# Optimization experiments

Hardware: AMD Instinct MI355X
Metric: run time of the kernel (lower is better)

The kernel has to match this reference:

```python
import jax, jax.numpy as jnp
import numpy as np

B, F, N = 16, 64, 32768
C0, C1, C2 = 64, 16, 1
TOP_K = 64
EPS = 1e-5


def setup_inputs() -> dict:
    key = jax.random.key(0)
    ks = jax.random.split(key, 6)
    def rn(k, shape, scale=1.0):
        return jax.random.normal(k, shape, dtype=jnp.float32) * scale
    return {
        "sortvec": rn(ks[0], (B, 1, F, N)),
        "input": rn(ks[1], (B, F, N)),
        # conv0: kernel (F,1), in=1, out=64 -> weight reduces to [C0, F]
        "w0": rn(ks[2], (C0, F), np.sqrt(2.0 / F)), "b0": jnp.zeros((C0,), jnp.float32),
        "w1": rn(ks[3], (C1, C0), np.sqrt(2.0 / C0)), "b1": jnp.zeros((C1,), jnp.float32),
        "w2": rn(ks[4], (C2, C1), np.sqrt(2.0 / C1)), "b2": jnp.zeros((C2,), jnp.float32),
        "g0": jnp.ones((C0,), jnp.float32), "bt0": jnp.zeros((C0,), jnp.float32),
        "g1": jnp.ones((C1,), jnp.float32), "bt1": jnp.zeros((C1,), jnp.float32),
        "g2": jnp.ones((C2,), jnp.float32), "bt2": jnp.zeros((C2,), jnp.float32),
    }


def _bn_relu(x, g, b):
    # training-mode BatchNorm2d over (B, N) per channel; x: [B, C, N]
    mu = jnp.mean(x, axis=(0, 2), keepdims=True)
    var = jnp.var(x, axis=(0, 2), keepdims=True)
    return jax.nn.relu((x - mu) * jax.lax.rsqrt(var + EPS) * g[None, :, None] + b[None, :, None])


def reference(sortvec, input, w0, b0, w1, b1, w2, b2, g0, bt0, g1, bt1, g2, bt2):
    # conv0 with kernel (F,1) collapses the feature axis: [B,1,F,N] -> [B,C0,N]
    x = jnp.einsum('bfn,of->bon', sortvec[:, 0], w0) + b0[None, :, None]
    x = _bn_relu(x, g0, bt0)
    x = _bn_relu(jnp.einsum('bcn,oc->bon', x, w1) + b1[None, :, None], g1, bt1)
    score = _bn_relu(jnp.einsum('bcn,oc->bon', x, w2) + b2[None, :, None], g2, bt2)  # [B,1,N]
    _, idx = jax.lax.top_k(score[:, 0], TOP_K)                                        # [B,K]
    sorted_input = jnp.take_along_axis(input, idx[:, None, :], axis=2)                # [B,F,K]
    sorted_score = jnp.take_along_axis(score, idx[:, None, :], axis=2)                # [B,1,K]
    feat = jnp.concatenate([sorted_input, sorted_score], axis=1)                      # [B,F+1,K]
    return feat, idx
```

## Files before the change

### kernel.cpp

```cpp
#include <hip/hip_runtime.h>


constexpr int   B_   = 16;
constexpr int   N_   = 32768;
constexpr int   K_   = 64;
constexpr long long S_ = (long long)B_ * N_;
constexpr float EPS_ = 1e-5f;

constexpr int NB0   = 1024;
constexpr int NB1   = 2048;
constexpr int NB2   = 128;
constexpr int T64   = 8192;
constexpr int NBINS = 4096;
constexpr int CAP   = 1024;

__device__ __forceinline__ unsigned key_map(float f) {
  unsigned u = __float_as_uint(f);
  return (u & 0x80000000u) ? ~u : (u | 0x80000000u);
}

__global__ __launch_bounds__(256) void k_prep(const float* __restrict__ w0,
                                              const float* __restrict__ w1,
                                              float* __restrict__ w0T,
                                              float* __restrict__ w1T) {
  int t = threadIdx.x;
  for (int e = t; e < 64 * 64; e += 256) {
    int o = e >> 6, f = e & 63;
    w0T[f * 64 + o] = w0[e];
  }
  for (int e = t; e < 16 * 64; e += 256) {
    int o = e >> 6, c = e & 63;
    w1T[c * 16 + o] = w1[e];
  }
}

__global__ __launch_bounds__(256) void k_stat0(const float* __restrict__ sv,
                                               const float* __restrict__ w0T,
                                               const float* __restrict__ b0,
                                               float* __restrict__ p0) {
  __shared__ float svt[64][64];
  const int t  = threadIdx.x;
  const int p  = t & 63;
  const int cg = __builtin_amdgcn_readfirstlane(t >> 6);

  float bb[16];
#pragma unroll
  for (int j = 0; j < 16; ++j) bb[j] = b0[cg * 16 + j];

  float s1[16], s2[16];
#pragma unroll
  for (int j = 0; j < 16; ++j) { s1[j] = 0.f; s2[j] = 0.f; }

  for (int tile = blockIdx.x; tile < T64; tile += NB0) {
    const int b  = tile >> 9;
    const int n0 = (tile & 511) << 6;
    const float* src = sv + ((long long)b * 64) * N_ + n0;
    __syncthreads();
#pragma unroll
    for (int q = 0; q < 4; ++q) {
      int e = t + q * 256;
      int f = e >> 4, c4 = (e & 15) << 2;
      *(float4*)&svt[f][c4] = *(const float4*)(src + (long long)f * N_ + c4);
    }
    __syncthreads();

    float y[16];
#pragma unroll
    for (int j = 0; j < 16; ++j) y[j] = bb[j];
    for (int f = 0; f < 64; ++f) {
      float s = svt[f][p];
      const float* wr = w0T + f * 64 + cg * 16;
#pragma unroll
      for (int j = 0; j < 16; ++j) y[j] = fmaf(wr[j], s, y[j]);
    }
#pragma unroll
    for (int j = 0; j < 16; ++j) {
      s1[j] += y[j];
      s2[j] = fmaf(y[j], y[j], s2[j]);
    }
  }

#pragma unroll
  for (int j = 0; j < 16; ++j) {
#pragma unroll
    for (int off = 32; off; off >>= 1) {
      s1[j] += __shfl_down(s1[j], off, 64);
      s2[j] += __shfl_down(s2[j], off, 64);
    }
  }
  if (p == 0) {
    float* dst = p0 + (long long)blockIdx.x * 128;
#pragma unroll
    for (int j = 0; j < 16; ++j) {
      dst[cg * 16 + j]      = s1[j];
      dst[64 + cg * 16 + j] = s2[j];
    }
  }
}

__global__ __launch_bounds__(128) void k_reduce0(const float* __restrict__ p0,
                                                 const float* __restrict__ g,
                                                 const float* __restrict__ bt,
                                                 float* __restrict__ st) {
  __shared__ float l[128];
  int j = threadIdx.x;
  float a0 = 0.f, a1 = 0.f, a2 = 0.f, a3 = 0.f;
  for (int i = 0; i < NB0; i += 4) {
    a0 += p0[(long long)(i + 0) * 128 + j];
    a1 += p0[(long long)(i + 1) * 128 + j];
    a2 += p0[(long long)(i + 2) * 128 + j];
    a3 += p0[(long long)(i + 3) * 128 + j];
  }
  l[j] = (a0 + a1) + (a2 + a3);
  __syncthreads();
  if (j < 64) {
    const float inv = 1.f / (float)S_;
    float mean = l[j] * inv;
    float ex2  = l[64 + j] * inv;
    float var  = ex2 - mean * mean;
    float sc   = g[j] * rsqrtf(var + EPS_);
    st[j]      = sc;
    st[64 + j] = bt[j] - mean * sc;
  }
}

__global__ __launch_bounds__(256) void k_layer01(const float* __restrict__ sv,
                                                 const float* __restrict__ w0T,
                                                 const float* __restrict__ b0,
                                                 const float* __restrict__ st0,
                                                 const float* __restrict__ w1T,
                                                 const float* __restrict__ b1,
                                                 float* __restrict__ y1,
                                                 float* __restrict__ p1) {
  __shared__ float svt[64][64];
  __shared__ float h0[64][64];
  const int t  = threadIdx.x;
  const int p  = t & 63;
  const int cg = __builtin_amdgcn_readfirstlane(t >> 6);

  float bb[16], sc[16], sh[16];
#pragma unroll
  for (int j = 0; j < 16; ++j) {
    bb[j] = b0[cg * 16 + j];
    sc[j] = st0[cg * 16 + j];
    sh[j] = st0[64 + cg * 16 + j];
  }
  float bb1[4];
#pragma unroll
  for (int j = 0; j < 4; ++j) bb1[j] = b1[cg * 4 + j];

  float s1[4], s2[4];
#pragma unroll
  for (int j = 0; j < 4; ++j) { s1[j] = 0.f; s2[j] = 0.f; }

  for (int tile = blockIdx.x; tile < T64; tile += NB1) {
    const int b  = tile >> 9;
    const int n0 = (tile & 511) << 6;
    const float* src = sv + ((long long)b * 64) * N_ + n0;
    __syncthreads();
#pragma unroll
    for (int q = 0; q < 4; ++q) {
      int e = t + q * 256;
      int f = e >> 4, c4 = (e & 15) << 2;
      *(float4*)&svt[f][c4] = *(const float4*)(src + (long long)f * N_ + c4);
    }
    __syncthreads();

    float y[16];
#pragma unroll
    for (int j = 0; j < 16; ++j) y[j] = bb[j];
    for (int f = 0; f < 64; ++f) {
      float s = svt[f][p];
      const float* wr = w0T + f * 64 + cg * 16;
#pragma unroll
      for (int j = 0; j < 16; ++j) y[j] = fmaf(wr[j], s, y[j]);
    }
#pragma unroll
    for (int j = 0; j < 16; ++j) {
      float h = fmaf(y[j], sc[j], sh[j]);
      h0[cg * 16 + j][p] = h > 0.f ? h : 0.f;
    }
    __syncthreads();

    float z[4];
#pragma unroll
    for (int j = 0; j < 4; ++j) z[j] = bb1[j];
    for (int f = 0; f < 64; ++f) {
      float h = h0[f][p];
      const float* wr = w1T + f * 16 + cg * 4;
#pragma unroll
      for (int j = 0; j < 4; ++j) z[j] = fmaf(wr[j], h, z[j]);
    }
#pragma unroll
    for (int j = 0; j < 4; ++j) {
      s1[j] += z[j];
      s2[j] = fmaf(z[j], z[j], s2[j]);
      y1[((long long)b * 16 + cg * 4 + j) * N_ + n0 + p] = z[j];
    }
  }

#pragma unroll
  for (int j = 0; j < 4; ++j) {
#pragma unroll
    for (int off = 32; off; off >>= 1) {
      s1[j] += __shfl_down(s1[j], off, 64);
      s2[j] += __shfl_down(s2[j], off, 64);
    }
  }
  if (p == 0) {
    float* dst = p1 + (long long)blockIdx.x * 32;
#pragma unroll
    for (int j = 0; j < 4; ++j) {
      dst[cg * 4 + j]      = s1[j];
      dst[16 + cg * 4 + j] = s2[j];
    }
  }
}

__global__ __launch_bounds__(64) void k_reduce1(const float* __restrict__ p1,
                                                const float* __restrict__ g,
                                                const float* __restrict__ bt,
                                                float* __restrict__ st) {
  __shared__ float l[32];
  int j = threadIdx.x;
  if (j < 32) {
    float a0 = 0.f, a1 = 0.f, a2 = 0.f, a3 = 0.f;
    for (int i = 0; i < NB1; i += 4) {
      a0 += p1[(long long)(i + 0) * 32 + j];
      a1 += p1[(long long)(i + 1) * 32 + j];
      a2 += p1[(long long)(i + 2) * 32 + j];
      a3 += p1[(long long)(i + 3) * 32 + j];
    }
    l[j] = (a0 + a1) + (a2 + a3);
  }
  __syncthreads();
  if (j < 16) {
    const float inv = 1.f / (float)S_;
    float mean = l[j] * inv;
    float ex2  = l[16 + j] * inv;
    float var  = ex2 - mean * mean;
    float sc   = g[j] * rsqrtf(var + EPS_);
    st[j]      = sc;
    st[16 + j] = bt[j] - mean * sc;
  }
}

__global__ __launch_bounds__(1024) void k_layer2(const float* __restrict__ y1,
                                                 const float* __restrict__ st1,
                                                 const float* __restrict__ w2,
                                                 const float* __restrict__ b2,
                                                 float* __restrict__ y2,
                                                 float* __restrict__ p2,
                                                 int* __restrict__ ghist) {
  __shared__ int hist[NBINS];
  __shared__ float ls[16], lq[16];
  const int t   = threadIdx.x;
  const int blk = blockIdx.x;
  const int b   = blk >> 3;
  const int n0  = ((blk & 7) << 12) | (t << 2);

#pragma unroll
  for (int i = 0; i < NBINS / 1024; ++i) hist[t + i * 1024] = 0;

  float sc[16], sh[16], w[16];
#pragma unroll
  for (int c = 0; c < 16; ++c) { sc[c] = st1[c]; sh[c] = st1[16 + c]; w[c] = w2[c]; }
  const float bias = b2[0];

  float a0 = bias, a1 = bias, a2 = bias, a3 = bias;
  const float* base = y1 + ((long long)b * 16) * N_ + n0;
#pragma unroll
  for (int c = 0; c < 16; ++c) {
    float4 v = *(const float4*)(base + (long long)c * N_);
    float h;
    h = fmaf(v.x, sc[c], sh[c]); h = h > 0.f ? h : 0.f; a0 = fmaf(w[c], h, a0);
    h = fmaf(v.y, sc[c], sh[c]); h = h > 0.f ? h : 0.f; a1 = fmaf(w[c], h, a1);
    h = fmaf(v.z, sc[c], sh[c]); h = h > 0.f ? h : 0.f; a2 = fmaf(w[c], h, a2);
    h = fmaf(v.w, sc[c], sh[c]); h = h > 0.f ? h : 0.f; a3 = fmaf(w[c], h, a3);
  }
  float4 o; o.x = a0; o.y = a1; o.z = a2; o.w = a3;
  *(float4*)(y2 + (long long)b * N_ + n0) = o;

  __syncthreads();

  atomicAdd(&hist[key_map(a0) >> 20], 1);
  atomicAdd(&hist[key_map(a1) >> 20], 1);
  atomicAdd(&hist[key_map(a2) >> 20], 1);
  atomicAdd(&hist[key_map(a3) >> 20], 1);

  float ss = (a0 + a1) + (a2 + a3);
  float sq = fmaf(a0, a0, fmaf(a1, a1, fmaf(a2, a2, a3 * a3)));
#pragma unroll
  for (int off = 32; off; off >>= 1) {
    ss += __shfl_down(ss, off, 64);
    sq += __shfl_down(sq, off, 64);
  }
  const int wid = t >> 6, lid = t & 63;
  if (lid == 0) { ls[wid] = ss; lq[wid] = sq; }
  __syncthreads();
  if (t == 0) {
    float Sv = 0.f, Qv = 0.f;
#pragma unroll
    for (int i = 0; i < 16; ++i) { Sv += ls[i]; Qv += lq[i]; }
    p2[blk * 2 + 0] = Sv;
    p2[blk * 2 + 1] = Qv;
  }
#pragma unroll
  for (int i = 0; i < NBINS / 1024; ++i) {
    int v = hist[t + i * 1024];
    if (v) atomicAdd(&ghist[b * NBINS + t + i * 1024], v);
  }
}

__global__ __launch_bounds__(256) void k_thresh(const int* __restrict__ ghist,
                                                int* __restrict__ Tb) {
  __shared__ int hl[NBINS + NBINS / 64];
  const int t = threadIdx.x, b = blockIdx.x;
  const int* h = ghist + b * NBINS;
  for (int i = t; i < NBINS; i += 256) hl[i + (i >> 6)] = h[i];
  __syncthreads();
  if (t < 64) {
    const int l = t;
    int s = 0;
    for (int j = 0; j < 64; ++j) s += hl[(l * 64 + j) + l];
    int Sv = s;
#pragma unroll
    for (int off = 1; off < 64; off <<= 1) {
      int v = __shfl_down(Sv, off, 64);
      if (l + off < 64) Sv += v;
    }
    unsigned long long m = __ballot(Sv >= K_);
    const int lstar = 63 - __builtin_clzll(m);
    const int tailS = (lstar < 63) ? __shfl(Sv, lstar + 1, 64) : 0;
    int Tj = hl[(lstar * 64 + l) + lstar];
#pragma unroll
    for (int off = 1; off < 64; off <<= 1) {
      int v = __shfl_down(Tj, off, 64);
      if (l + off < 64) Tj += v;
    }
    const int cge = Tj + tailS;
    unsigned long long m2 = __ballot(cge >= K_);
    const int jstar = 63 - __builtin_clzll(m2);
    if (l == 0) Tb[b] = lstar * 64 + jstar;
  }
}

__global__ __launch_bounds__(1024) void k_compact(const float* __restrict__ y2,
                                                  const int* __restrict__ Tb,
                                                  int* __restrict__ cnt,
                                                  unsigned long long* __restrict__ cand) {
  const int t = threadIdx.x, blk = blockIdx.x;
  const int b  = blk >> 3;
  const int n0 = ((blk & 7) << 12) | (t << 2);
  const int T  = Tb[b];
  float4 v = *(const float4*)(y2 + (long long)b * N_ + n0);
  unsigned long long* cb = cand + (long long)b * CAP;
#define DO_CAND(comp, off)                                                    \
  {                                                                           \
    unsigned u = key_map(comp);                                               \
    if ((int)(u >> 20) >= T) {                                                \
      int slot = atomicAdd(&cnt[b], 1);                                       \
      if (slot < CAP)                                                         \
        cb[slot] = ((unsigned long long)u << 32) |                            \
                   (unsigned)(N_ - 1 - (n0 + off));                           \
    }                                                                         \
  }
  DO_CAND(v.x, 0) DO_CAND(v.y, 1) DO_CAND(v.z, 2) DO_CAND(v.w, 3)
#undef DO_CAND
}

__global__ __launch_bounds__(64) void k_final(const unsigned long long* __restrict__ cand,
                                              const int* __restrict__ cnt,
                                              const float* __restrict__ p2,
                                              const float* __restrict__ g2,
                                              const float* __restrict__ bt2,
                                              const float* __restrict__ inp,
                                              float* __restrict__ out) {
  const int b = blockIdx.x, l = threadIdx.x;

  float s1 = p2[2 * l] + p2[2 * (l + 64)];
  float q1 = p2[2 * l + 1] + p2[2 * (l + 64) + 1];
#pragma unroll
  for (int off = 32; off; off >>= 1) {
    s1 += __shfl_down(s1, off, 64);
    q1 += __shfl_down(q1, off, 64);
  }
  s1 = __shfl(s1, 0, 64);
  q1 = __shfl(q1, 0, 64);
  const float inv = 1.f / (float)S_;
  const float mean = s1 * inv;
  const float var  = q1 * inv - mean * mean;
  const float scale2 = g2[0] * rsqrtf(var + EPS_);
  const float shift2 = bt2[0] - mean * scale2;

  int cn = cnt[b];
  if (cn > CAP) cn = CAP;
  const unsigned long long* cb = cand + (long long)b * CAP;
  unsigned long long k[16];
#pragma unroll
  for (int r = 0; r < 16; ++r) {
    int i = l + r * 64;
    k[r] = (i < cn) ? cb[i] : 0ull;
  }
  unsigned long long cur = 0ull;
#pragma unroll
  for (int r = 0; r < 16; ++r) cur = k[r] > cur ? k[r] : cur;

  int myidx = 0;
  unsigned mymap = 0;
  for (int r = 0; r < K_; ++r) {
    unsigned long long m = cur;
#pragma unroll
    for (int off = 32; off; off >>= 1) {
      unsigned long long o = __shfl_xor(m, off, 64);
      m = o > m ? o : m;
    }
    if (r == l) {
      myidx = N_ - 1 - (int)(m & 0xffffffffu);
      mymap = (unsigned)(m >> 32);
    }
    if (cur == m) {
#pragma unroll
      for (int r2 = 0; r2 < 16; ++r2)
        if (k[r2] == m) k[r2] = 0ull;
      unsigned long long c2 = 0ull;
#pragma unroll
      for (int r2 = 0; r2 < 16; ++r2) c2 = k[r2] > c2 ? k[r2] : c2;
      cur = c2;
    }
  }

  unsigned u = mymap;
  u = (u & 0x80000000u) ? (u & 0x7fffffffu) : ~u;
  float v = __uint_as_float(u);
  float scv = fmaf(v, scale2, shift2);
  scv = scv > 0.f ? scv : 0.f;

  const float* ib = inp + ((long long)b * 64) * N_;
#pragma unroll 4
  for (int f = 0; f < 64; ++f)
    out[((long long)b * 65 + f) * 64 + l] = ib[(long long)f * N_ + myidx];
  out[((long long)b * 65 + 64) * 64 + l] = scv;
  out[(long long)B_ * 65 * 64 + b * 64 + l] = (float)myidx;
}

extern "C" void kernel_launch(void* const* d_in, const int* in_sizes, int n_in,
                              void* d_out, int out_size, void* d_ws, size_t ws_size,
                              hipStream_t stream) {
  const float* sv  = (const float*)d_in[0];
  const float* inp = (const float*)d_in[1];
  const float* w0  = (const float*)d_in[2];
  const float* b0  = (const float*)d_in[3];
  const float* w1  = (const float*)d_in[4];
  const float* b1  = (const float*)d_in[5];
  const float* w2  = (const float*)d_in[6];
  const float* b2  = (const float*)d_in[7];
  const float* g0  = (const float*)d_in[8];
  const float* bt0 = (const float*)d_in[9];
  const float* g1  = (const float*)d_in[10];
  const float* bt1 = (const float*)d_in[11];
  const float* g2  = (const float*)d_in[12];
  const float* bt2 = (const float*)d_in[13];
  float* out = (float*)d_out;

  float* ws  = (float*)d_ws;
  float* y1  = ws;
  float* y2  = y1 + (size_t)S_ * 16;
  float* p0  = y2 + (size_t)S_;
  float* p1  = p0 + (size_t)NB0 * 128;
  float* p2  = p1 + (size_t)NB1 * 32;
  float* st0 = p2 + 256;
  float* st1 = st0 + 128;
  float* w0T = st1 + 32;
  float* w1T = w0T + 4096;
  int*   ghist = (int*)(w1T + 1024);
  int*   cnt   = ghist + (size_t)B_ * NBINS;
  int*   Tb    = cnt + 16;
  unsigned long long* cand =
      (unsigned long long*)(Tb + 16);

  hipMemsetAsync(ghist, 0, ((size_t)B_ * NBINS + 16) * sizeof(int), stream);

  k_prep   <<<1,    256, 0, stream>>>(w0, w1, w0T, w1T);
  k_stat0  <<<NB0,  256, 0, stream>>>(sv, w0T, b0, p0);
  k_reduce0<<<1,    128, 0, stream>>>(p0, g0, bt0, st0);
  k_layer01<<<NB1,  256, 0, stream>>>(sv, w0T, b0, st0, w1T, b1, y1, p1);
  k_reduce1<<<1,     64, 0, stream>>>(p1, g1, bt1, st1);
  k_layer2 <<<NB2, 1024, 0, stream>>>(y1, st1, w2, b2, y2, p2, ghist);
  k_thresh <<<B_,   256, 0, stream>>>(ghist, Tb);
  k_compact<<<NB2, 1024, 0, stream>>>(y2, Tb, cnt, cand);
  k_final  <<<B_,    64, 0, stream>>>(cand, cnt, p2, g2, bt2, inp, out);
}
```

Measured before the change: 279.6 us.

## Restructure layer0/1 kernels to one position per thread with register accumulation

```diff
diff --git a/kernel.cpp b/kernel.cpp
--- a/kernel.cpp
+++ b/kernel.cpp
@@ -7,10 +7,11 @@
 constexpr long long S_ = (long long)B_ * N_;
 constexpr float EPS_ = 1e-5f;
 
-constexpr int NB0   = 1024;
+constexpr int NBA   = 512;
+constexpr int PA_POS = 8;
 constexpr int NB1   = 2048;
-constexpr int NB2   = 128;
-constexpr int T64   = 8192;
+constexpr int NB2   = 256;
+constexpr int NBC   = 128;
 constexpr int NBINS = 4096;
 constexpr int CAP   = 1024;
 
@@ -38,64 +39,60 @@
                                                const float* __restrict__ w0T,
                                                const float* __restrict__ b0,
                                                float* __restrict__ p0) {
-  __shared__ float svt[64][64];
-  const int t  = threadIdx.x;
-  const int p  = t & 63;
-  const int cg = __builtin_amdgcn_readfirstlane(t >> 6);
-
-  float bb[16];
-#pragma unroll
-  for (int j = 0; j < 16; ++j) bb[j] = b0[cg * 16 + j];
-
-  float s1[16], s2[16];
-#pragma unroll
-  for (int j = 0; j < 16; ++j) { s1[j] = 0.f; s2[j] = 0.f; }
-
-  for (int tile = blockIdx.x; tile < T64; tile += NB0) {
-    const int b  = tile >> 9;
-    const int n0 = (tile & 511) << 6;
-    const float* src = sv + ((long long)b * 64) * N_ + n0;
-    __syncthreads();
-#pragma unroll
-    for (int q = 0; q < 4; ++q) {
-      int e = t + q * 256;
-      int f = e >> 4, c4 = (e & 15) << 2;
-      *(float4*)&svt[f][c4] = *(const float4*)(src + (long long)f * N_ + c4);
-    }
-    __syncthreads();
-
-    float y[16];
-#pragma unroll
-    for (int j = 0; j < 16; ++j) y[j] = bb[j];
+  __shared__ float red[4][64];
+  const int t    = threadIdx.x;
+  const int blk  = blockIdx.x;
+  const int half = blk & 1;
+  const int pb   = blk >> 1;
+  const int c0   = half * 32;
+
+  float bb[32];
+#pragma unroll
+  for (int c = 0; c < 32; ++c) bb[c] = b0[c0 + c];
+
+  float s1[32], s2[32];
+#pragma unroll
+  for (int c = 0; c < 32; ++c) { s1[c] = 0.f; s2[c] = 0.f; }
+
+  const long long pbase = (long long)pb * 2048 + t;
+  for (int i = 0; i < PA_POS; ++i) {
+    const long long pos = pbase + i * 256;
+    const int b = (int)(pos >> 15);
+    const int n = (int)(pos & (N_ - 1));
+    const float* xp = sv + ((long long)b * 64) * N_ + n;
+    float y[32];
+#pragma unroll
+    for (int c = 0; c < 32; ++c) y[c] = bb[c];
+#pragma unroll
     for (int f = 0; f < 64; ++f) {
-      float s = svt[f][p];
-      const float* wr = w0T + f * 64 + cg * 16;
-#pragma unroll
-      for (int j = 0; j < 16; ++j) y[j] = fmaf(wr[j], s, y[j]);
-    }
-#pragma unroll
-    for (int j = 0; j < 16; ++j) {
-      s1[j] += y[j];
-      s2[j] = fmaf(y[j], y[j], s2[j]);
-    }
-  }
-
-#pragma unroll
-  for (int j = 0; j < 16; ++j) {
+      float x = xp[(long long)f * N_];
+      const float* wr = w0T + f * 64 + c0;
+#pragma unroll
+      for (int c = 0; c < 32; ++c) y[c] = fmaf(wr[c], x, y[c]);
+    }
+#pragma unroll
+    for (int c = 0; c < 32; ++c) {
+      s1[c] += y[c];
+      s2[c] = fmaf(y[c], y[c], s2[c]);
+    }
+  }
+
+#pragma unroll
+  for (int c = 0; c < 32; ++c) {
 #pragma unroll
     for (int off = 32; off; off >>= 1) {
-      s1[j] += __shfl_down(s1[j], off, 64);
-      s2[j] += __shfl_down(s2[j], off, 64);
-    }
-  }
-  if (p == 0) {
-    float* dst = p0 + (long long)blockIdx.x * 128;
-#pragma unroll
-    for (int j = 0; j < 16; ++j) {
-      dst[cg * 16 + j]      = s1[j];
-      dst[64 + cg * 16 + j] = s2[j];
-    }
-  }
+      s1[c] += __shfl_down(s1[c], off, 64);
+      s2[c] += __shfl_down(s2[c], off, 64);
+    }
+  }
+  const int wid = t >> 6, lid = t & 63;
+  if (lid == 0) {
+#pragma unroll
+    for (int c = 0; c < 32; ++c) { red[wid][c] = s1[c]; red[wid][32 + c] = s2[c]; }
+  }
+  __syncthreads();
+  if (t < 64)
+    p0[blk * 64 + t] = (red[0][t] + red[1][t]) + (red[2][t] + red[3][t]);
 }
 
 __global__ __launch_bounds__(128) void k_reduce0(const float* __restrict__ p0,
@@ -103,15 +100,14 @@
                                                  const float* __restrict__ bt,
                                                  float* __restrict__ st) {
   __shared__ float l[128];
-  int j = threadIdx.x;
-  float a0 = 0.f, a1 = 0.f, a2 = 0.f, a3 = 0.f;
-  for (int i = 0; i < NB0; i += 4) {
-    a0 += p0[(long long)(i + 0) * 128 + j];
-    a1 += p0[(long long)(i + 1) * 128 + j];
-    a2 += p0[(long long)(i + 2) * 128 + j];
-    a3 += p0[(long long)(i + 3) * 128 + j];
-  }
-  l[j] = (a0 + a1) + (a2 + a3);
+  const int j    = threadIdx.x;
+  const int stat = j >> 6;
+  const int ch   = j & 63;
+  const int half = ch >> 5, c = ch & 31;
+  float a = 0.f;
+  for (int pb = 0; pb < 256; ++pb)
+    a += p0[(pb * 2 + half) * 64 + stat * 32 + c];
+  l[j] = a;
   __syncthreads();
   if (j < 64) {
     const float inv = 1.f / (float)S_;
@@ -132,89 +128,58 @@
                                                  const float* __restrict__ b1,
                                                  float* __restrict__ y1,
                                                  float* __restrict__ p1) {
-  __shared__ float svt[64][64];
-  __shared__ float h0[64][64];
-  const int t  = threadIdx.x;
-  const int p  = t & 63;
-  const int cg = __builtin_amdgcn_readfirstlane(t >> 6);
-
-  float bb[16], sc[16], sh[16];
+  __shared__ float red[4][32];
+  const int t   = threadIdx.x;
+  const int blk = blockIdx.x;
+  const long long pos = (long long)blk * 256 + t;
+  const int b = (int)(pos >> 15);
+  const int n = (int)(pos & (N_ - 1));
+  const float* xp = sv + ((long long)b * 64) * N_ + n;
+
+  float y[64];
+#pragma unroll
+  for (int c = 0; c < 64; ++c) y[c] = b0[c];
+#pragma unroll
+  for (int f = 0; f < 64; ++f) {
+    float x = xp[(long long)f * N_];
+    const float* wr = w0T + f * 64;
+#pragma unroll
+    for (int c = 0; c < 64; ++c) y[c] = fmaf(wr[c], x, y[c]);
+  }
+#pragma unroll
+  for (int c = 0; c < 64; ++c) {
+    float h = fmaf(y[c], st0[c], st0[64 + c]);
+    y[c] = h > 0.f ? h : 0.f;
+  }
+
+  float z[16];
+#pragma unroll
+  for (int j = 0; j < 16; ++j) z[j] = b1[j];
+#pragma unroll
+  for (int f = 0; f < 64; ++f) {
+    const float* wr = w1T + f * 16;
+#pragma unroll
+    for (int j = 0; j < 16; ++j) z[j] = fmaf(wr[j], y[f], z[j]);
+  }
+
+  float* yo = y1 + ((long long)b * 16) * N_ + n;
+#pragma unroll
+  for (int j = 0; j < 16; ++j) yo[(long long)j * N_] = z[j];
+
+  const int wid = t >> 6, lid = t & 63;
 #pragma unroll
   for (int j = 0; j < 16; ++j) {
-    bb[j] = b0[cg * 16 + j];
-    sc[j] = st0[cg * 16 + j];
-    sh[j] = st0[64 + cg * 16 + j];
-  }
-  float bb1[4];
-#pragma unroll
-  for (int j = 0; j < 4; ++j) bb1[j] = b1[cg * 4 + j];
-
-  float s1[4], s2[4];
-#pragma unroll
-  for (int j = 0; j < 4; ++j) { s1[j] = 0.f; s2[j] = 0.f; }
-
-  for (int tile = blockIdx.x; tile < T64; tile += NB1) {
-    const int b  = tile >> 9;
-    const int n0 = (tile & 511) << 6;
-    const float* src = sv + ((long long)b * 64) * N_ + n0;
-    __syncthreads();
-#pragma unroll
-    for (int q = 0; q < 4; ++q) {
-      int e = t + q * 256;
-      int f = e >> 4, c4 = (e & 15) << 2;
-      *(float4*)&svt[f][c4] = *(const float4*)(src + (long long)f * N_ + c4);
-    }
-    __syncthreads();
-
-    float y[16];
-#pragma unroll
-    for (int j = 0; j < 16; ++j) y[j] = bb[j];
-    for (int f = 0; f < 64; ++f) {
-      float s = svt[f][p];
-      const float* wr = w0T + f * 64 + cg * 16;
-#pragma unroll
-      for (int j = 0; j < 16; ++j) y[j] = fmaf(wr[j], s, y[j]);
-    }
-#pragma unroll
-    for (int j = 0; j < 16; ++j) {
-      float h = fmaf(y[j], sc[j], sh[j]);
-      h0[cg * 16 + j][p] = h > 0.f ? h : 0.f;
-    }
-    __syncthreads();
-
-    float z[4];
-#pragma unroll
-    for (int j = 0; j < 4; ++j) z[j] = bb1[j];
-    for (int f = 0; f < 64; ++f) {
-      float h = h0[f][p];
-      const float* wr = w1T + f * 16 + cg * 4;
-#pragma unroll
-      for (int j = 0; j < 4; ++j) z[j] = fmaf(wr[j], h, z[j]);
-    }
-#pragma unroll
-    for (int j = 0; j < 4; ++j) {
-      s1[j] += z[j];
-      s2[j] = fmaf(z[j], z[j], s2[j]);
-      y1[((long long)b * 16 + cg * 4 + j) * N_ + n0 + p] = z[j];
-    }
-  }
-
-#pragma unroll
-  for (int j = 0; j < 4; ++j) {
+    float a = z[j], q = z[j] * z[j];
 #pragma unroll
     for (int off = 32; off; off >>= 1) {
-      s1[j] += __shfl_down(s1[j], off, 64);
-      s2[j] += __shfl_down(s2[j], off, 64);
-    }
-  }
-  if (p == 0) {
-    float* dst = p1 + (long long)blockIdx.x * 32;
-#pragma unroll
-    for (int j = 0; j < 4; ++j) {
-      dst[cg * 4 + j]      = s1[j];
-      dst[16 + cg * 4 + j] = s2[j];
-    }
-  }
+      a += __shfl_down(a, off, 64);
+      q += __shfl_down(q, off, 64);
+    }
+    if (lid == 0) { red[wid][j] = a; red[wid][16 + j] = q; }
+  }
+  __syncthreads();
+  if (t < 32)
+    p1[blk * 32 + t] = (red[0][t] + red[1][t]) + (red[2][t] + red[3][t]);
 }
 
 __global__ __launch_bounds__(64) void k_reduce1(const float* __restrict__ p1,
@@ -256,8 +221,8 @@
   __shared__ float ls[16], lq[16];
   const int t   = threadIdx.x;
   const int blk = blockIdx.x;
-  const int b   = blk >> 3;
-  const int n0  = ((blk & 7) << 12) | (t << 2);
+  const int b   = blk >> 4;
+  const int n0  = ((blk & 15) << 11) | (t << 1);
 
 #pragma unroll
   for (int i = 0; i < NBINS / 1024; ++i) hist[t + i * 1024] = 0;
@@ -267,29 +232,25 @@
   for (int c = 0; c < 16; ++c) { sc[c] = st1[c]; sh[c] = st1[16 + c]; w[c] = w2[c]; }
   const float bias = b2[0];
 
-  float a0 = bias, a1 = bias, a2 = bias, a3 = bias;
+  float a0 = bias, a1 = bias;
   const float* base = y1 + ((long long)b * 16) * N_ + n0;
 #pragma unroll
   for (int c = 0; c < 16; ++c) {
-    float4 v = *(const float4*)(base + (long long)c * N_);
+    float2 v = *(const float2*)(base + (long long)c * N_);
     float h;
     h = fmaf(v.x, sc[c], sh[c]); h = h > 0.f ? h : 0.f; a0 = fmaf(w[c], h, a0);
     h = fmaf(v.y, sc[c], sh[c]); h = h > 0.f ? h : 0.f; a1 = fmaf(w[c], h, a1);
-    h = fmaf(v.z, sc[c], sh[c]); h = h > 0.f ? h : 0.f; a2 = fmaf(w[c], h, a2);
-    h = fmaf(v.w, sc[c], sh[c]); h = h > 0.f ? h : 0.f; a3 = fmaf(w[c], h, a3);
-  }
-  float4 o; o.x = a0; o.y = a1; o.z = a2; o.w = a3;
-  *(float4*)(y2 + (long long)b * N_ + n0) = o;
+  }
+  float2 o; o.x = a0; o.y = a1;
+  *(float2*)(y2 + (long long)b * N_ + n0) = o;
 
   __syncthreads();
 
   atomicAdd(&hist[key_map(a0) >> 20], 1);
   atomicAdd(&hist[key_map(a1) >> 20], 1);
-  atomicAdd(&hist[key_map(a2) >> 20], 1);
-  atomicAdd(&hist[key_map(a3) >> 20], 1);
-
-  float ss = (a0 + a1) + (a2 + a3);
-  float sq = fmaf(a0, a0, fmaf(a1, a1, fmaf(a2, a2, a3 * a3)));
+
+  float ss = a0 + a1;
+  float sq = fmaf(a0, a0, a1 * a1);
 #pragma unroll
   for (int off = 32; off; off >>= 1) {
     ss += __shfl_down(ss, off, 64);
@@ -378,8 +339,10 @@
                                               float* __restrict__ out) {
   const int b = blockIdx.x, l = threadIdx.x;
 
-  float s1 = p2[2 * l] + p2[2 * (l + 64)];
-  float q1 = p2[2 * l + 1] + p2[2 * (l + 64) + 1];
+  float s1 = (p2[2 * l] + p2[2 * (l + 64)]) +
+             (p2[2 * (l + 128)] + p2[2 * (l + 192)]);
+  float q1 = (p2[2 * l + 1] + p2[2 * (l + 64) + 1]) +
+             (p2[2 * (l + 128) + 1] + p2[2 * (l + 192) + 1]);
 #pragma unroll
   for (int off = 32; off; off >>= 1) {
     s1 += __shfl_down(s1, off, 64);
@@ -467,9 +430,9 @@
   float* y1  = ws;
   float* y2  = y1 + (size_t)S_ * 16;
   float* p0  = y2 + (size_t)S_;
-  float* p1  = p0 + (size_t)NB0 * 128;
+  float* p1  = p0 + (size_t)NBA * 64;
   float* p2  = p1 + (size_t)NB1 * 32;
-  float* st0 = p2 + 256;
+  float* st0 = p2 + (size_t)NB2 * 2;
   float* st1 = st0 + 128;
   float* w0T = st1 + 32;
   float* w1T = w0T + 4096;
@@ -482,12 +445,12 @@
   hipMemsetAsync(ghist, 0, ((size_t)B_ * NBINS + 16) * sizeof(int), stream);
 
   k_prep   <<<1,    256, 0, stream>>>(w0, w1, w0T, w1T);
-  k_stat0  <<<NB0,  256, 0, stream>>>(sv, w0T, b0, p0);
+  k_stat0  <<<NBA,  256, 0, stream>>>(sv, w0T, b0, p0);
   k_reduce0<<<1,    128, 0, stream>>>(p0, g0, bt0, st0);
   k_layer01<<<NB1,  256, 0, stream>>>(sv, w0T, b0, st0, w1T, b1, y1, p1);
   k_reduce1<<<1,     64, 0, stream>>>(p1, g1, bt1, st1);
   k_layer2 <<<NB2, 1024, 0, stream>>>(y1, st1, w2, b2, y2, p2, ghist);
   k_thresh <<<B_,   256, 0, stream>>>(ghist, Tb);
-  k_compact<<<NB2, 1024, 0, stream>>>(y2, Tb, cnt, cand);
+  k_compact<<<NBC, 1024, 0, stream>>>(y2, Tb, cnt, cand);
   k_final  <<<B_,    64, 0, stream>>>(cand, cnt, p2, g2, bt2, inp, out);
 }
```

Result: slower. 581.4 us (+108.0%).

## Materialize conv0 output to avoid recomputing first layer in layer01 pass

Applied to the files above, without the earlier changes.

```diff
diff --git a/kernel.cpp b/kernel.cpp
--- a/kernel.cpp
+++ b/kernel.cpp
@@ -8,9 +8,11 @@
 constexpr float EPS_ = 1e-5f;
 
 constexpr int NB0   = 1024;
+constexpr int T64   = 8192;
+constexpr int NBN1  = 512;
 constexpr int NB1   = 2048;
-constexpr int NB2   = 128;
-constexpr int T64   = 8192;
+constexpr int NB2   = 256;
+constexpr int NBC   = 128;
 constexpr int NBINS = 4096;
 constexpr int CAP   = 1024;
 
@@ -34,9 +36,11 @@
   }
 }
 
-__global__ __launch_bounds__(256) void k_stat0(const float* __restrict__ sv,
+template <bool STORE_Y0>
+__global__ __launch_bounds__(256) void k_conv0(const float* __restrict__ sv,
                                                const float* __restrict__ w0T,
                                                const float* __restrict__ b0,
+                                               float* __restrict__ y0,
                                                float* __restrict__ p0) {
   __shared__ float svt[64][64];
   const int t  = threadIdx.x;
@@ -78,6 +82,11 @@
       s1[j] += y[j];
       s2[j] = fmaf(y[j], y[j], s2[j]);
     }
+    if constexpr (STORE_Y0) {
+      float* dst = y0 + ((long long)(b * 64 + cg * 16)) * N_ + n0 + p;
+#pragma unroll
+      for (int j = 0; j < 16; ++j) dst[(long long)j * N_] = y[j];
+    }
   }
 
 #pragma unroll
@@ -101,11 +110,12 @@
 __global__ __launch_bounds__(128) void k_reduce0(const float* __restrict__ p0,
                                                  const float* __restrict__ g,
                                                  const float* __restrict__ bt,
-                                                 float* __restrict__ st) {
+                                                 float* __restrict__ st,
+                                                 int nb) {
   __shared__ float l[128];
   int j = threadIdx.x;
   float a0 = 0.f, a1 = 0.f, a2 = 0.f, a3 = 0.f;
-  for (int i = 0; i < NB0; i += 4) {
+  for (int i = 0; i < nb; i += 4) {
     a0 += p0[(long long)(i + 0) * 128 + j];
     a1 += p0[(long long)(i + 1) * 128 + j];
     a2 += p0[(long long)(i + 2) * 128 + j];
@@ -122,6 +132,64 @@
     st[j]      = sc;
     st[64 + j] = bt[j] - mean * sc;
   }
+}
+
+__global__ __launch_bounds__(256) void k_bn1(const float* __restrict__ y0,
+                                             const float* __restrict__ st0,
+                                             const float* __restrict__ w1T,
+                                             const float* __restrict__ b1,
+                                             float* __restrict__ y1,
+                                             float* __restrict__ p1) {
+  __shared__ float red[4][32];
+  const int t = threadIdx.x;
+
+  float s1[16], s2[16];
+#pragma unroll
+  for (int j = 0; j < 16; ++j) { s1[j] = 0.f; s2[j] = 0.f; }
+
+  for (int tile = blockIdx.x; tile < 2048; tile += NBN1) {
+    const long long pos = (long long)tile * 256 + t;
+    const int b = (int)(pos >> 15);
+    const int n = (int)(pos & (N_ - 1));
+    const float* xp = y0 + ((long long)b * 64) * N_ + n;
+
+    float z[16];
+#pragma unroll
+    for (int j = 0; j < 16; ++j) z[j] = b1[j];
+#pragma unroll 8
+    for (int c = 0; c < 64; ++c) {
+      float v = xp[(long long)c * N_];
+      float h = fmaf(v, st0[c], st0[64 + c]);
+      h = h > 0.f ? h : 0.f;
+      const float* wr = w1T + c * 16;
+#pragma unroll
+      for (int j = 0; j < 16; ++j) z[j] = fmaf(wr[j], h, z[j]);
+    }
+
+    float* yo = y1 + ((long long)b * 16) * N_ + n;
+#pragma unroll
+    for (int j = 0; j < 16; ++j) {
+      yo[(long long)j * N_] = z[j];
+      s1[j] += z[j];
+      s2[j] = fmaf(z[j], z[j], s2[j]);
+    }
+  }
+
+  const int wid = t >> 6, lid = t & 63;
+#pragma unroll
+  for (int j = 0; j < 16; ++j) {
+    float a = s1[j], q = s2[j];
+#pragma unroll
+    for (int off = 32; off; off >>= 1) {
+      a += __shfl_down(a, off, 64);
+      q += __shfl_down(q, off, 64);
+    }
+    if (lid == 0) { red[wid][j] = a; red[wid][16 + j] = q; }
+  }
+  __syncthreads();
+  if (t < 32)
+    p1[(long long)blockIdx.x * 32 + t] =
+        (red[0][t] + red[1][t]) + (red[2][t] + red[3][t]);
 }
 
 __global__ __launch_bounds__(256) void k_layer01(const float* __restrict__ sv,
@@ -220,12 +288,13 @@
 __global__ __launch_bounds__(64) void k_reduce1(const float* __restrict__ p1,
                                                 const float* __restrict__ g,
                                                 const float* __restrict__ bt,
-                                                float* __restrict__ st) {
+                                                float* __restrict__ st,
+                                                int nb) {
   __shared__ float l[32];
   int j = threadIdx.x;
   if (j < 32) {
     float a0 = 0.f, a1 = 0.f, a2 = 0.f, a3 = 0.f;
-    for (int i = 0; i < NB1; i += 4) {
+    for (int i = 0; i < nb; i += 4) {
       a0 += p1[(long long)(i + 0) * 32 + j];
       a1 += p1[(long long)(i + 1) * 32 + j];
       a2 += p1[(long long)(i + 2) * 32 + j];
@@ -256,8 +325,8 @@
   __shared__ float ls[16], lq[16];
   const int t   = threadIdx.x;
   const int blk = blockIdx.x;
-  const int b   = blk >> 3;
-  const int n0  = ((blk & 7) << 12) | (t << 2);
+  const int b   = blk >> 4;
+  const int n0  = ((blk & 15) << 11) | (t << 1);
 
 #pragma unroll
   for (int i = 0; i < NBINS / 1024; ++i) hist[t + i * 1024] = 0;
@@ -267,29 +336,25 @@
   for (int c = 0; c < 16; ++c) { sc[c] = st1[c]; sh[c] = st1[16 + c]; w[c] = w2[c]; }
   const float bias = b2[0];
 
-  float a0 = bias, a1 = bias, a2 = bias, a3 = bias;
+  float a0 = bias, a1 = bias;
   const float* base = y1 + ((long long)b * 16) * N_ + n0;
 #pragma unroll
   for (int c = 0; c < 16; ++c) {
-    float4 v = *(const float4*)(base + (long long)c * N_);
+    float2 v = *(const float2*)(base + (long long)c * N_);
     float h;
     h = fmaf(v.x, sc[c], sh[c]); h = h > 0.f ? h : 0.f; a0 = fmaf(w[c], h, a0);
     h = fmaf(v.y, sc[c], sh[c]); h = h > 0.f ? h : 0.f; a1 = fmaf(w[c], h, a1);
-    h = fmaf(v.z, sc[c], sh[c]); h = h > 0.f ? h : 0.f; a2 = fmaf(w[c], h, a2);
-    h = fmaf(v.w, sc[c], sh[c]); h = h > 0.f ? h : 0.f; a3 = fmaf(w[c], h, a3);
-  }
-  float4 o; o.x = a0; o.y = a1; o.z = a2; o.w = a3;
-  *(float4*)(y2 + (long long)b * N_ + n0) = o;
+  }
+  float2 o; o.x = a0; o.y = a1;
+  *(float2*)(y2 + (long long)b * N_ + n0) = o;
 
   __syncthreads();
 
   atomicAdd(&hist[key_map(a0) >> 20], 1);
   atomicAdd(&hist[key_map(a1) >> 20], 1);
-  atomicAdd(&hist[key_map(a2) >> 20], 1);
-  atomicAdd(&hist[key_map(a3) >> 20], 1);
-
-  float ss = (a0 + a1) + (a2 + a3);
-  float sq = fmaf(a0, a0, fmaf(a1, a1, fmaf(a2, a2, a3 * a3)));
+
+  float ss = a0 + a1;
+  float sq = fmaf(a0, a0, a1 * a1);
 #pragma unroll
   for (int off = 32; off; off >>= 1) {
     ss += __shfl_down(ss, off, 64);
@@ -378,8 +443,10 @@
                                               float* __restrict__ out) {
   const int b = blockIdx.x, l = threadIdx.x;
 
-  float s1 = p2[2 * l] + p2[2 * (l + 64)];
-  float q1 = p2[2 * l + 1] + p2[2 * (l + 64) + 1];
+  float s1 = (p2[2 * l] + p2[2 * (l + 64)]) +
+             (p2[2 * (l + 128)] + p2[2 * (l + 192)]);
+  float q1 = (p2[2 * l + 1] + p2[2 * (l + 64) + 1]) +
+             (p2[2 * (l + 128) + 1] + p2[2 * (l + 192) + 1]);
 #pragma unroll
   for (int off = 32; off; off >>= 1) {
     s1 += __shfl_down(s1, off, 64);
@@ -469,7 +536,7 @@
   float* p0  = y2 + (size_t)S_;
   float* p1  = p0 + (size_t)NB0 * 128;
   float* p2  = p1 + (size_t)NB1 * 32;
-  float* st0 = p2 + 256;
+  float* st0 = p2 + (size_t)NB2 * 2;
   float* st1 = st0 + 128;
   float* w0T = st1 + 32;
   float* w1T = w0T + 4096;
@@ -478,16 +545,30 @@
   int*   Tb    = cnt + 16;
   unsigned long long* cand =
       (unsigned long long*)(Tb + 16);
+  float* y0 = (float*)(cand + (size_t)B_ * CAP);
+
+  const size_t need_bytes =
+      (size_t)((const char*)(y0 + (size_t)S_ * 64) - (const char*)d_ws);
+  const bool store_path = ws_size >= need_bytes;
 
   hipMemsetAsync(ghist, 0, ((size_t)B_ * NBINS + 16) * sizeof(int), stream);
 
-  k_prep   <<<1,    256, 0, stream>>>(w0, w1, w0T, w1T);
-  k_stat0  <<<NB0,  256, 0, stream>>>(sv, w0T, b0, p0);
-  k_reduce0<<<1,    128, 0, stream>>>(p0, g0, bt0, st0);
-  k_layer01<<<NB1,  256, 0, stream>>>(sv, w0T, b0, st0, w1T, b1, y1, p1);
-  k_reduce1<<<1,     64, 0, stream>>>(p1, g1, bt1, st1);
+  k_prep<<<1, 256, 0, stream>>>(w0, w1, w0T, w1T);
+
+  if (store_path) {
+    k_conv0<true><<<NB0, 256, 0, stream>>>(sv, w0T, b0, y0, p0);
+    k_reduce0<<<1, 128, 0, stream>>>(p0, g0, bt0, st0, NB0);
+    k_bn1<<<NBN1, 256, 0, stream>>>(y0, st0, w1T, b1, y1, p1);
+    k_reduce1<<<1, 64, 0, stream>>>(p1, g1, bt1, st1, NBN1);
+  } else {
+    k_conv0<false><<<NB0, 256, 0, stream>>>(sv, w0T, b0, nullptr, p0);
+    k_reduce0<<<1, 128, 0, stream>>>(p0, g0, bt0, st0, NB0);
+    k_layer01<<<NB1, 256, 0, stream>>>(sv, w0T, b0, st0, w1T, b1, y1, p1);
+    k_reduce1<<<1, 64, 0, stream>>>(p1, g1, bt1, st1, NB1);
+  }
+
   k_layer2 <<<NB2, 1024, 0, stream>>>(y1, st1, w2, b2, y2, p2, ghist);
   k_thresh <<<B_,   256, 0, stream>>>(ghist, Tb);
-  k_compact<<<NB2, 1024, 0, stream>>>(y2, Tb, cnt, cand);
+  k_compact<<<NBC, 1024, 0, stream>>>(y2, Tb, cnt, cand);
   k_final  <<<B_,    64, 0, stream>>>(cand, cnt, p2, g2, bt2, inp, out);
 }
```

Result: slower. 305.7 us (+9.3%).

## Widen tiles to 128 columns with two points per thread and parallelize BN reductions

Applied to the files above, without the earlier changes.

```diff
diff --git a/kernel.cpp b/kernel.cpp
--- a/kernel.cpp
+++ b/kernel.cpp
@@ -7,10 +7,11 @@
 constexpr long long S_ = (long long)B_ * N_;
 constexpr float EPS_ = 1e-5f;
 
-constexpr int NB0   = 1024;
+constexpr int T128  = 4096;
+constexpr int NB0   = 2048;
 constexpr int NB1   = 2048;
-constexpr int NB2   = 128;
-constexpr int T64   = 8192;
+constexpr int NB2   = 256;
+constexpr int NBC   = 128;
 constexpr int NBINS = 4096;
 constexpr int CAP   = 1024;
 
@@ -38,7 +39,7 @@
                                                const float* __restrict__ w0T,
                                                const float* __restrict__ b0,
                                                float* __restrict__ p0) {
-  __shared__ float svt[64][64];
+  __shared__ float svt[64][128];
   const int t  = threadIdx.x;
   const int p  = t & 63;
   const int cg = __builtin_amdgcn_readfirstlane(t >> 6);
@@ -51,32 +52,35 @@
 #pragma unroll
   for (int j = 0; j < 16; ++j) { s1[j] = 0.f; s2[j] = 0.f; }
 
-  for (int tile = blockIdx.x; tile < T64; tile += NB0) {
-    const int b  = tile >> 9;
-    const int n0 = (tile & 511) << 6;
+  for (int tile = blockIdx.x; tile < T128; tile += NB0) {
+    const int b  = tile >> 8;
+    const int n0 = (tile & 255) << 7;
     const float* src = sv + ((long long)b * 64) * N_ + n0;
     __syncthreads();
 #pragma unroll
-    for (int q = 0; q < 4; ++q) {
+    for (int q = 0; q < 8; ++q) {
       int e = t + q * 256;
-      int f = e >> 4, c4 = (e & 15) << 2;
+      int f = e >> 5, c4 = (e & 31) << 2;
       *(float4*)&svt[f][c4] = *(const float4*)(src + (long long)f * N_ + c4);
     }
     __syncthreads();
 
-    float y[16];
-#pragma unroll
-    for (int j = 0; j < 16; ++j) y[j] = bb[j];
+    float2 y[16];
+#pragma unroll
+    for (int j = 0; j < 16; ++j) { y[j].x = bb[j]; y[j].y = bb[j]; }
     for (int f = 0; f < 64; ++f) {
-      float s = svt[f][p];
+      const float2 x = *(const float2*)&svt[f][p << 1];
       const float* wr = w0T + f * 64 + cg * 16;
 #pragma unroll
-      for (int j = 0; j < 16; ++j) y[j] = fmaf(wr[j], s, y[j]);
+      for (int j = 0; j < 16; ++j) {
+        y[j].x = fmaf(wr[j], x.x, y[j].x);
+        y[j].y = fmaf(wr[j], x.y, y[j].y);
+      }
     }
 #pragma unroll
     for (int j = 0; j < 16; ++j) {
-      s1[j] += y[j];
-      s2[j] = fmaf(y[j], y[j], s2[j]);
+      s1[j] += y[j].x + y[j].y;
+      s2[j] = fmaf(y[j].x, y[j].x, fmaf(y[j].y, y[j].y, s2[j]));
     }
   }
 
@@ -98,29 +102,36 @@
   }
 }
 
-__global__ __launch_bounds__(128) void k_reduce0(const float* __restrict__ p0,
-                                                 const float* __restrict__ g,
-                                                 const float* __restrict__ bt,
-                                                 float* __restrict__ st) {
-  __shared__ float l[128];
-  int j = threadIdx.x;
+__global__ __launch_bounds__(1024) void k_reduce0(const float* __restrict__ p0,
+                                                  const float* __restrict__ g,
+                                                  const float* __restrict__ bt,
+                                                  float* __restrict__ st) {
+  __shared__ float l[8][128];
+  const int t = threadIdx.x;
+  const int j = t & 127, grp = t >> 7;
   float a0 = 0.f, a1 = 0.f, a2 = 0.f, a3 = 0.f;
-  for (int i = 0; i < NB0; i += 4) {
-    a0 += p0[(long long)(i + 0) * 128 + j];
-    a1 += p0[(long long)(i + 1) * 128 + j];
-    a2 += p0[(long long)(i + 2) * 128 + j];
-    a3 += p0[(long long)(i + 3) * 128 + j];
-  }
-  l[j] = (a0 + a1) + (a2 + a3);
-  __syncthreads();
-  if (j < 64) {
+  for (int i = grp; i < 512; i += 8) {
+    a0 += p0[(long long)i * 128 + j];
+    a1 += p0[(long long)(i + 512) * 128 + j];
+    a2 += p0[(long long)(i + 1024) * 128 + j];
+    a3 += p0[(long long)(i + 1536) * 128 + j];
+  }
+  l[grp][j] = (a0 + a1) + (a2 + a3);
+  __syncthreads();
+  if (t < 128) {
+    float v = ((l[0][t] + l[1][t]) + (l[2][t] + l[3][t])) +
+              ((l[4][t] + l[5][t]) + (l[6][t] + l[7][t]));
+    l[0][t] = v;
+  }
+  __syncthreads();
+  if (t < 64) {
     const float inv = 1.f / (float)S_;
-    float mean = l[j] * inv;
-    float ex2  = l[64 + j] * inv;
+    float mean = l[0][t] * inv;
+    float ex2  = l[0][64 + t] * inv;
     float var  = ex2 - mean * mean;
-    float sc   = g[j] * rsqrtf(var + EPS_);
-    st[j]      = sc;
-    st[64 + j] = bt[j] - mean * sc;
+    float sc   = g[t] * rsqrtf(var + EPS_);
+    st[t]      = sc;
+    st[64 + t] = bt[t] - mean * sc;
   }
 }
 
@@ -132,8 +143,7 @@
                                                  const float* __restrict__ b1,
                                                  float* __restrict__ y1,
                                                  float* __restrict__ p1) {
-  __shared__ float svt[64][64];
-  __shared__ float h0[64][64];
+  __shared__ float buf[64][128];
   const int t  = threadIdx.x;
   const int p  = t & 63;
   const int cg = __builtin_amdgcn_readfirstlane(t >> 6);
@@ -149,53 +159,65 @@
 #pragma unroll
   for (int j = 0; j < 4; ++j) bb1[j] = b1[cg * 4 + j];
 
-  float s1[4], s2[4];
-#pragma unroll
-  for (int j = 0; j < 4; ++j) { s1[j] = 0.f; s2[j] = 0.f; }
-
-  for (int tile = blockIdx.x; tile < T64; tile += NB1) {
-    const int b  = tile >> 9;
-    const int n0 = (tile & 511) << 6;
+  float sA[4], qA[4];
+#pragma unroll
+  for (int j = 0; j < 4; ++j) { sA[j] = 0.f; qA[j] = 0.f; }
+
+  for (int tile = blockIdx.x; tile < T128; tile += NB1) {
+    const int b  = tile >> 8;
+    const int n0 = (tile & 255) << 7;
     const float* src = sv + ((long long)b * 64) * N_ + n0;
     __syncthreads();
 #pragma unroll
-    for (int q = 0; q < 4; ++q) {
+    for (int q = 0; q < 8; ++q) {
       int e = t + q * 256;
-      int f = e >> 4, c4 = (e & 15) << 2;
-      *(float4*)&svt[f][c4] = *(const float4*)(src + (long long)f * N_ + c4);
+      int f = e >> 5, c4 = (e & 31) << 2;
+      *(float4*)&buf[f][c4] = *(const float4*)(src + (long long)f * N_ + c4);
     }
     __syncthreads();
 
-    float y[16];
-#pragma unroll
-    for (int j = 0; j < 16; ++j) y[j] = bb[j];
+    float2 y[16];
+#pragma unroll
+    for (int j = 0; j < 16; ++j) { y[j].x = bb[j]; y[j].y = bb[j]; }
     for (int f = 0; f < 64; ++f) {
-      float s = svt[f][p];
+      const float2 x = *(const float2*)&buf[f][p << 1];
       const float* wr = w0T + f * 64 + cg * 16;
 #pragma unroll
-      for (int j = 0; j < 16; ++j) y[j] = fmaf(wr[j], s, y[j]);
-    }
+      for (int j = 0; j < 16; ++j) {
+        y[j].x = fmaf(wr[j], x.x, y[j].x);
+        y[j].y = fmaf(wr[j], x.y, y[j].y);
+      }
+    }
+    __syncthreads();
+
 #pragma unroll
     for (int j = 0; j < 16; ++j) {
-      float h = fmaf(y[j], sc[j], sh[j]);
-      h0[cg * 16 + j][p] = h > 0.f ? h : 0.f;
+      float2 h;
+      h.x = fmaf(y[j].x, sc[j], sh[j]); h.x = h.x > 0.f ? h.x : 0.f;
+      h.y = fmaf(y[j].y, sc[j], sh[j]); h.y = h.y > 0.f ? h.y : 0.f;
+      *(float2*)&buf[cg * 16 + j][p << 1] = h;
     }
     __syncthreads();
 
-    float z[4];
-#pragma unroll
-    for (int j = 0; j < 4; ++j) z[j] = bb1[j];
-    for (int f = 0; f < 64; ++f) {
-      float h = h0[f][p];
-      const float* wr = w1T + f * 16 + cg * 4;
-#pragma unroll
-      for (int j = 0; j < 4; ++j) z[j] = fmaf(wr[j], h, z[j]);
-    }
+    float2 z[4];
+#pragma unroll
+    for (int j = 0; j < 4; ++j) { z[j].x = bb1[j]; z[j].y = bb1[j]; }
+    for (int c = 0; c < 64; ++c) {
+      const float2 h = *(const float2*)&buf[c][p << 1];
+      const float* wr = w1T + c * 16 + cg * 4;
+#pragma unroll
+      for (int j = 0; j < 4; ++j) {
+        z[j].x = fmaf(wr[j], h.x, z[j].x);
+        z[j].y = fmaf(wr[j], h.y, z[j].y);
+      }
+    }
+
+    float* yo = y1 + ((long long)(b * 16 + cg * 4)) * N_ + n0 + (p << 1);
 #pragma unroll
     for (int j = 0; j < 4; ++j) {
-      s1[j] += z[j];
-      s2[j] = fmaf(z[j], z[j], s2[j]);
-      y1[((long long)b * 16 + cg * 4 + j) * N_ + n0 + p] = z[j];
+      *(float2*)(yo + (long long)j * N_) = z[j];
+      sA[j] += z[j].x + z[j].y;
+      qA[j] = fmaf(z[j].x, z[j].x, fmaf(z[j].y, z[j].y, qA[j]));
     }
   }
 
@@ -203,45 +225,49 @@
   for (int j = 0; j < 4; ++j) {
 #pragma unroll
     for (int off = 32; off; off >>= 1) {
-      s1[j] += __shfl_down(s1[j], off, 64);
-      s2[j] += __shfl_down(s2[j], off, 64);
+      sA[j] += __shfl_down(sA[j], off, 64);
+      qA[j] += __shfl_down(qA[j], off, 64);
     }
   }
   if (p == 0) {
     float* dst = p1 + (long long)blockIdx.x * 32;
 #pragma unroll
     for (int j = 0; j < 4; ++j) {
-      dst[cg * 4 + j]      = s1[j];
-      dst[16 + cg * 4 + j] = s2[j];
-    }
-  }
-}
-
-__global__ __launch_bounds__(64) void k_reduce1(const float* __restrict__ p1,
-                                                const float* __restrict__ g,
-                                                const float* __restrict__ bt,
-                                                float* __restrict__ st) {
-  __shared__ float l[32];
-  int j = threadIdx.x;
-  if (j < 32) {
-    float a0 = 0.f, a1 = 0.f, a2 = 0.f, a3 = 0.f;
-    for (int i = 0; i < NB1; i += 4) {
-      a0 += p1[(long long)(i + 0) * 32 + j];
-      a1 += p1[(long long)(i + 1) * 32 + j];
-      a2 += p1[(long long)(i + 2) * 32 + j];
-      a3 += p1[(long long)(i + 3) * 32 + j];
-    }
-    l[j] = (a0 + a1) + (a2 + a3);
-  }
-  __syncthreads();
-  if (j < 16) {
+      dst[cg * 4 + j]      = sA[j];
+      dst[16 + cg * 4 + j] = qA[j];
+    }
+  }
+}
+
+__global__ __launch_bounds__(1024) void k_reduce1(const float* __restrict__ p1,
+                                                  const float* __restrict__ g,
+                                                  const float* __restrict__ bt,
+                                                  float* __restrict__ st) {
+  __shared__ float l[32][32];
+  const int t = threadIdx.x;
+  const int j = t & 31, grp = t >> 5;
+  float a0 = 0.f, a1 = 0.f;
+  for (int i = grp; i < 1024; i += 32) {
+    a0 += p1[(long long)i * 32 + j];
+    a1 += p1[(long long)(i + 1024) * 32 + j];
+  }
+  l[grp][j] = a0 + a1;
+  __syncthreads();
+  if (t < 32) {
+    float v = 0.f;
+#pragma unroll
+    for (int g2 = 0; g2 < 32; ++g2) v += l[g2][t];
+    l[0][t] = v;
+  }
+  __syncthreads();
+  if (t < 16) {
     const float inv = 1.f / (float)S_;
-    float mean = l[j] * inv;
-    float ex2  = l[16 + j] * inv;
+    float mean = l[0][t] * inv;
+    float ex2  = l[0][16 + t] * inv;
     float var  = ex2 - mean * mean;
-    float sc   = g[j] * rsqrtf(var + EPS_);
-    st[j]      = sc;
-    st[16 + j] = bt[j] - mean * sc;
+    float sc   = g[t] * rsqrtf(var + EPS_);
+    st[t]      = sc;
+    st[16 + t] = bt[t] - mean * sc;
   }
 }
 
@@ -256,8 +282,8 @@
   __shared__ float ls[16], lq[16];
   const int t   = threadIdx.x;
   const int blk = blockIdx.x;
-  const int b   = blk >> 3;
-  const int n0  = ((blk & 7) << 12) | (t << 2);
+  const int b   = blk >> 4;
+  const int n0  = ((blk & 15) << 11) | (t << 1);
 
 #pragma unroll
   for (int i = 0; i < NBINS / 1024; ++i) hist[t + i * 1024] = 0;
@@ -267,29 +293,25 @@
   for (int c = 0; c < 16; ++c) { sc[c] = st1[c]; sh[c] = st1[16 + c]; w[c] = w2[c]; }
   const float bias = b2[0];
 
-  float a0 = bias, a1 = bias, a2 = bias, a3 = bias;
+  float a0 = bias, a1 = bias;
   const float* base = y1 + ((long long)b * 16) * N_ + n0;
 #pragma unroll
   for (int c = 0; c < 16; ++c) {
-    float4 v = *(const float4*)(base + (long long)c * N_);
+    float2 v = *(const float2*)(base + (long long)c * N_);
     float h;
     h = fmaf(v.x, sc[c], sh[c]); h = h > 0.f ? h : 0.f; a0 = fmaf(w[c], h, a0);
     h = fmaf(v.y, sc[c], sh[c]); h = h > 0.f ? h : 0.f; a1 = fmaf(w[c], h, a1);
-    h = fmaf(v.z, sc[c], sh[c]); h = h > 0.f ? h : 0.f; a2 = fmaf(w[c], h, a2);
-    h = fmaf(v.w, sc[c], sh[c]); h = h > 0.f ? h : 0.f; a3 = fmaf(w[c], h, a3);
-  }
-  float4 o; o.x = a0; o.y = a1; o.z = a2; o.w = a3;
-  *(float4*)(y2 + (long long)b * N_ + n0) = o;
+  }
+  float2 o; o.x = a0; o.y = a1;
+  *(float2*)(y2 + (long long)b * N_ + n0) = o;
 
   __syncthreads();
 
   atomicAdd(&hist[key_map(a0) >> 20], 1);
   atomicAdd(&hist[key_map(a1) >> 20], 1);
-  atomicAdd(&hist[key_map(a2) >> 20], 1);
-  atomicAdd(&hist[key_map(a3) >> 20], 1);
-
-  float ss = (a0 + a1) + (a2 + a3);
-  float sq = fmaf(a0, a0, fmaf(a1, a1, fmaf(a2, a2, a3 * a3)));
+
+  float ss = a0 + a1;
+  float sq = fmaf(a0, a0, a1 * a1);
 #pragma unroll
   for (int off = 32; off; off >>= 1) {
     ss += __shfl_down(ss, off, 64);
@@ -378,8 +400,10 @@
                                               float* __restrict__ out) {
   const int b = blockIdx.x, l = threadIdx.x;
 
-  float s1 = p2[2 * l] + p2[2 * (l + 64)];
-  float q1 = p2[2 * l + 1] + p2[2 * (l + 64) + 1];
+  float s1 = (p2[2 * l] + p2[2 * (l + 64)]) +
+             (p2[2 * (l + 128)] + p2[2 * (l + 192)]);
+  float q1 = (p2[2 * l + 1] + p2[2 * (l + 64) + 1]) +
+             (p2[2 * (l + 128) + 1] + p2[2 * (l + 192) + 1]);
 #pragma unroll
   for (int off = 32; off; off >>= 1) {
     s1 += __shfl_down(s1, off, 64);
@@ -469,7 +493,7 @@
   float* p0  = y2 + (size_t)S_;
   float* p1  = p0 + (size_t)NB0 * 128;
   float* p2  = p1 + (size_t)NB1 * 32;
-  float* st0 = p2 + 256;
+  float* st0 = p2 + (size_t)NB2 * 2;
   float* st1 = st0 + 128;
   float* w0T = st1 + 32;
   float* w1T = w0T + 4096;
@@ -483,11 +507,11 @@
 
   k_prep   <<<1,    256, 0, stream>>>(w0, w1, w0T, w1T);
   k_stat0  <<<NB0,  256, 0, stream>>>(sv, w0T, b0, p0);
-  k_reduce0<<<1,    128, 0, stream>>>(p0, g0, bt0, st0);
+  k_reduce0<<<1,   1024, 0, stream>>>(p0, g0, bt0, st0);
   k_layer01<<<NB1,  256, 0, stream>>>(sv, w0T, b0, st0, w1T, b1, y1, p1);
-  k_reduce1<<<1,     64, 0, stream>>>(p1, g1, bt1, st1);
+  k_reduce1<<<1,   1024, 0, stream>>>(p1, g1, bt1, st1);
   k_layer2 <<<NB2, 1024, 0, stream>>>(y1, st1, w2, b2, y2, p2, ghist);
   k_thresh <<<B_,   256, 0, stream>>>(ghist, Tb);
-  k_compact<<<NB2, 1024, 0, stream>>>(y2, Tb, cnt, cand);
+  k_compact<<<NBC, 1024, 0, stream>>>(y2, Tb, cnt, cand);
   k_final  <<<B_,    64, 0, stream>>>(cand, cnt, p2, g2, bt2, inp, out);
 }
```

After: 292.8 us. 4.7% more time.
